# Performance work log

Hardware: AMD Instinct MI355X
Metric: run time of the kernel (lower is better)

Reference implementation:

```python
import jax, jax.numpy as jnp
import numpy as np

G = 56          # voxel grid resolution per axis
N = 65536
K = 27          # 3x3x3 kernel offsets
C_IN = 128
C_OUT = 128


def _build_rulebook():
    """Submanifold conv rulebook: for each kernel offset, (input_row, output_row) pairs.

    Padded to P=N pairs per offset; invalid pairs use in_idx=0 and out_idx=N
    (a dummy output slot that is dropped), so shapes are static.
    """
    rng = np.random.default_rng(0)
    keys = np.sort(rng.choice(G ** 3, size=N, replace=False)).astype(np.int64)
    x = keys // (G * G)
    y = (keys // G) % G
    z = keys % G
    in_idx = np.zeros((K, N), dtype=np.int32)
    out_idx = np.full((K, N), N, dtype=np.int32)
    k = 0
    for dx in (-1, 0, 1):
        for dy in (-1, 0, 1):
            for dz in (-1, 0, 1):
                nx, ny, nz = x + dx, y + dy, z + dz
                valid = (nx >= 0) & (nx < G) & (ny >= 0) & (ny < G) & (nz >= 0) & (nz < G)
                nkey = (nx * G + ny) * G + nz
                pos = np.searchsorted(keys, np.clip(nkey, 0, G ** 3 - 1))
                pos = np.clip(pos, 0, N - 1)
                found = valid & (keys[pos] == nkey)
                cnt = int(found.sum())
                in_idx[k, :cnt] = pos[found]
                out_idx[k, :cnt] = np.nonzero(found)[0]
                k += 1
    return jnp.asarray(in_idx), jnp.asarray(out_idx)


def setup_inputs() -> dict:
    key = jax.random.key(0)
    k1, k2, k3 = jax.random.split(key, 3)
    fan_in = K * C_IN
    features = jax.random.normal(k1, (N, C_IN), dtype=jnp.float32)
    weight = jax.random.normal(k2, (K, C_IN, C_OUT), dtype=jnp.float32) * (1.0 / np.sqrt(fan_in))
    bias = jax.random.normal(k3, (C_OUT,), dtype=jnp.float32) * 0.01
    in_idx, out_idx = _build_rulebook()
    return {"features": features, "weight": weight, "bias": bias,
            "in_idx": in_idx, "out_idx": out_idx}


def reference(features, weight, bias, in_idx, out_idx):
    # gather: [K, P, C_in]
    gathered = features[in_idx]
    # per-offset GEMM: [K, P, C_out]
    contrib = jnp.einsum('kpc,kcd->kpd', gathered, weight)
    n = features.shape[0]
    c_out = weight.shape[-1]
    # scatter-accumulate into N real rows + 1 dummy row for padded pairs
    out = jnp.zeros((n + 1, c_out), dtype=features.dtype)
    out = out.at[out_idx.reshape(-1)].add(contrib.reshape(-1, c_out))
    return out[:n] + bias
```

## Files before the change

kernel.cpp:

```cpp
#include <hip/hip_runtime.h>
#include <hip/hip_bf16.h>
#include <stdint.h>

#define NV   65536
#define KOFF 27
#define CIN  128
#define COUT 128

typedef __bf16 bf16x8 __attribute__((ext_vector_type(8)));
typedef float  f32x4  __attribute__((ext_vector_type(4)));

__device__ __forceinline__ void async_copy16(void* lds, const void* g) {
    __builtin_amdgcn_global_load_lds(
        (const __attribute__((address_space(1))) void*)g,
        (__attribute__((address_space(3))) void*)lds,
        16, 0, 0);
}

#define JOB_A_BLOCKS 4097
#define JOB_B_BLOCKS 216
#define JOB_S_BLOCKS 1728

__global__ void k_prep_all(const float* __restrict__ f,
                           uint4* __restrict__ fb4,
                           const float* __restrict__ w,
                           uint4* __restrict__ wfrag4,
                           const int4* __restrict__ in4,
                           const int4* __restrict__ out4,
                           int* __restrict__ nbr) {
    const int b = blockIdx.x;
    const int t = threadIdx.x;
    if (b < JOB_A_BLOCKS) {
        int i = b * 256 + t;
        int total8  = (NV + 1) * CIN / 8;
        int nvalid8 = NV * CIN / 8;
        if (i >= total8) return;
        union { uint4 u; __hip_bfloat16 h[8]; } p;
        if (i < nvalid8) {
            const float4* f4 = (const float4*)f;
            float4 a = f4[i * 2];
            float4 c = f4[i * 2 + 1];
            p.h[0] = __float2bfloat16(a.x);
            p.h[1] = __float2bfloat16(a.y);
            p.h[2] = __float2bfloat16(a.z);
            p.h[3] = __float2bfloat16(a.w);
            p.h[4] = __float2bfloat16(c.x);
            p.h[5] = __float2bfloat16(c.y);
            p.h[6] = __float2bfloat16(c.z);
            p.h[7] = __float2bfloat16(c.w);
        } else {
            p.u = make_uint4(0, 0, 0, 0);
        }
        fb4[i] = p.u;
    } else if (b < JOB_A_BLOCKS + JOB_B_BLOCKS) {
        int c    = (b - JOB_A_BLOCKS) * 256 + t;
        int lane = c & 63;
        int nt   = (c >> 6) & 1;
        int ks   = (c >> 7) & 3;
        int wv   = (c >> 9) & 3;
        int k    = c >> 11;
        int cout = wv * 32 + nt * 16 + (lane & 15);
        int cin0 = ks * 32 + (lane >> 4) * 8;
        const float* wk = w + k * 16384;
        union { uint4 u; __hip_bfloat16 h[8]; } p;
        #pragma unroll
        for (int j = 0; j < 8; ++j)
            p.h[j] = __float2bfloat16(wk[(cin0 + j) * 128 + cout]);
        wfrag4[c] = p.u;
    } else {
        int i = (b - JOB_A_BLOCKS - JOB_B_BLOCKS) * 256 + t;
        int k = i >> 14;
        int4 ii = in4[i];
        int4 oo = out4[i];
        int* nb = nbr + k * (NV + 1);
        nb[oo.x] = ii.x;
        nb[oo.y] = ii.y;
        nb[oo.z] = ii.z;
        nb[oo.w] = ii.w;
    }
}

__global__ __launch_bounds__(256, 2)
void sp_conv_main(const __hip_bfloat16* __restrict__ feats,
                  const uint4* __restrict__ wfrag,
                  const int* __restrict__ nbr,
                  const float* __restrict__ bias,
                  float* __restrict__ out) {
    __shared__ unsigned char smem[65536];

    const int t   = threadIdx.x;
    const int bid = blockIdx.x;
    const int tile0 = ((bid & 7) * 64 + (bid >> 3)) * 128;

    const int w    = t >> 6;
    const int lane = t & 63;
    const int lr   = lane & 15;
    const int quad = lane >> 4;

    const int srow   = t >> 4;
    const int sbyte  = ((t & 15) ^ srow) * 16;

    f32x4 acc[8][2] = {};

    const unsigned char* featsB = (const unsigned char*)feats;

    int arows[8];
    {
        const int* nbr0 = nbr + tile0;
        #pragma unroll
        for (int i = 0; i < 8; ++i) arows[i] = nbr0[i * 16 + srow];
    }
    #pragma unroll
    for (int i = 0; i < 8; ++i) {
        unsigned ar = min((unsigned)arows[i], (unsigned)NV);
        async_copy16(smem + i * 4096 + t * 16,
                     featsB + (size_t)ar * 256 + sbyte);
    }
    {
        const int* nbr1 = nbr + (NV + 1) + tile0;
        #pragma unroll
        for (int i = 0; i < 8; ++i) arows[i] = nbr1[i * 16 + srow];
    }
    uint4 bcur[4][2], bnext[4][2];
    {
        const uint4* wf0 = wfrag + w * 512 + lane;
        #pragma unroll
        for (int ks = 0; ks < 4; ++ks)
            #pragma unroll
            for (int nt = 0; nt < 2; ++nt)
                bcur[ks][nt] = wf0[ks * 128 + nt * 64];
    }
    __syncthreads();

    int cbuf = 0;
    for (int k = 0; k < KOFF; ++k) {
        if (k + 1 < KOFF) {
            unsigned char* dst = smem + (cbuf ^ 1) * 32768;
            #pragma unroll
            for (int i = 0; i < 8; ++i) {
                unsigned ar = min((unsigned)arows[i], (unsigned)NV);
                async_copy16(dst + i * 4096 + t * 16,
                             featsB + (size_t)ar * 256 + sbyte);
            }
            if (k + 2 < KOFF) {
                const int* nbrn = nbr + (k + 2) * (NV + 1) + tile0;
                #pragma unroll
                for (int i = 0; i < 8; ++i) arows[i] = nbrn[i * 16 + srow];
            }
            const uint4* wfn = wfrag + (k + 1) * 2048 + w * 512 + lane;
            #pragma unroll
            for (int ks = 0; ks < 4; ++ks)
                #pragma unroll
                for (int nt = 0; nt < 2; ++nt)
                    bnext[ks][nt] = wfn[ks * 128 + nt * 64];
        }

        const unsigned char* base = smem + cbuf * 32768;
        #pragma unroll
        for (int ks = 0; ks < 4; ++ks) {
            bf16x8 af[8];
            #pragma unroll
            for (int mt = 0; mt < 8; ++mt) {
                int row = mt * 16 + lr;
                af[mt] = *(const bf16x8*)(base + row * 256 +
                                          (((ks * 4 + quad) ^ lr) * 16));
            }
            #pragma unroll
            for (int mt = 0; mt < 8; ++mt)
                #pragma unroll
                for (int nt = 0; nt < 2; ++nt)
                    acc[mt][nt] = __builtin_amdgcn_mfma_f32_16x16x32_bf16(
                        af[mt], *(const bf16x8*)&bcur[ks][nt],
                        acc[mt][nt], 0, 0, 0);
        }
        __syncthreads();
        #pragma unroll
        for (int ks = 0; ks < 4; ++ks)
            #pragma unroll
            for (int nt = 0; nt < 2; ++nt)
                bcur[ks][nt] = bnext[ks][nt];
        cbuf ^= 1;
    }

    const int n0w = w * 32;
    float bv[2];
    #pragma unroll
    for (int nt = 0; nt < 2; ++nt) bv[nt] = bias[n0w + nt * 16 + lr];

    #pragma unroll
    for (int mt = 0; mt < 8; ++mt) {
        #pragma unroll
        for (int nt = 0; nt < 2; ++nt) {
            #pragma unroll
            for (int r = 0; r < 4; ++r) {
                int grow = tile0 + mt * 16 + quad * 4 + r;
                out[(size_t)grow * COUT + n0w + nt * 16 + lr] =
                    acc[mt][nt][r] + bv[nt];
            }
        }
    }
}


extern "C" void kernel_launch(void* const* d_in, const int* in_sizes, int n_in,
                              void* d_out, int out_size, void* d_ws, size_t ws_size,
                              hipStream_t stream) {
    const float* features = (const float*)d_in[0];
    const float* weight   = (const float*)d_in[1];
    const float* bias     = (const float*)d_in[2];
    const int*   in_idx   = (const int*)d_in[3];
    const int*   out_idx  = (const int*)d_in[4];
    float* out = (float*)d_out;

    uint8_t* ws = (uint8_t*)d_ws;
    size_t off = 0;
    __hip_bfloat16* feats_bf = (__hip_bfloat16*)(ws + off);
    off += (size_t)(NV + 1) * CIN * 2;
    off = (off + 255) & ~(size_t)255;
    uint4* wfrag = (uint4*)(ws + off);
    off += (size_t)KOFF * CIN * COUT * 2;
    off = (off + 255) & ~(size_t)255;
    int* nbr = (int*)(ws + off);

    hipMemsetAsync(nbr, 0xFF, (size_t)KOFF * (NV + 1) * 4, stream);

    k_prep_all<<<JOB_A_BLOCKS + JOB_B_BLOCKS + JOB_S_BLOCKS, 256, 0, stream>>>(
        features, (uint4*)feats_bf, weight, wfrag,
        (const int4*)in_idx, (const int4*)out_idx, nbr);

    sp_conv_main<<<NV / 128, 256, 0, stream>>>(feats_bf, wfrag, nbr, bias, out);
}
```

Baseline: 158.2 us.

## Split kernel offsets across three blocks per tile with atomic accumulation

Splits the 27 kernel offsets into three groups of nine. Each output tile is now handled by three blocks that write their partial sums into a zeroed output with float atomicAdd, and the first group adds the bias. This triples the grid from 512 blocks, which is meant to fill the many CUs better. The feature tile drops to a single 32KB LDS buffer so three blocks can fit per CU, and weight fragments are reordered and prefetched per k-slice in place of double-buffering whole offsets. The cost is an extra memset of the output, atomic traffic on 32MB of output, and lost overlap between the gather and the compute.

```diff
diff --git a/kernel.cpp b/kernel.cpp
--- a/kernel.cpp
+++ b/kernel.cpp
@@ -6,6 +6,8 @@
 #define KOFF 27
 #define CIN  128
 #define COUT 128
+#define NGRP 3
+#define KPG  9
 
 typedef __bf16 bf16x8 __attribute__((ext_vector_type(8)));
 typedef float  f32x4  __attribute__((ext_vector_type(4)));
@@ -56,9 +58,10 @@
         int c    = (b - JOB_A_BLOCKS) * 256 + t;
         int lane = c & 63;
         int nt   = (c >> 6) & 1;
-        int ks   = (c >> 7) & 3;
-        int wv   = (c >> 9) & 3;
-        int k    = c >> 11;
+        int wv   = (c >> 7) & 3;
+        int s    = c >> 9;
+        int ks   = s & 3;
+        int k    = s >> 2;
         int cout = wv * 32 + nt * 16 + (lane & 15);
         int cin0 = ks * 32 + (lane >> 4) * 8;
         const float* wk = w + k * 16384;
@@ -80,89 +83,83 @@
     }
 }
 
-__global__ __launch_bounds__(256, 2)
+__global__ __launch_bounds__(256, 3)
 void sp_conv_main(const __hip_bfloat16* __restrict__ feats,
                   const uint4* __restrict__ wfrag,
                   const int* __restrict__ nbr,
                   const float* __restrict__ bias,
                   float* __restrict__ out) {
-    __shared__ unsigned char smem[65536];
+    __shared__ unsigned char smA[32768];
 
     const int t   = threadIdx.x;
     const int bid = blockIdx.x;
-    const int tile0 = ((bid & 7) * 64 + (bid >> 3)) * 128;
+    const int g   = bid % NGRP;
+    const int tb  = bid / NGRP;
+    const int tile0 = ((tb & 7) * 64 + (tb >> 3)) * 128;
+    const int kbeg  = g * KPG;
+    const int send  = (kbeg + KPG) * 4;
 
     const int w    = t >> 6;
     const int lane = t & 63;
     const int lr   = lane & 15;
     const int quad = lane >> 4;
+    const int n0w  = w * 32;
 
     const int srow   = t >> 4;
     const int sbyte  = ((t & 15) ^ srow) * 16;
 
-    f32x4 acc[8][2] = {};
+    f32x4 acc[8][2];
+    {
+        float b0 = (g == 0) ? bias[n0w + lr]      : 0.0f;
+        float b1 = (g == 0) ? bias[n0w + 16 + lr] : 0.0f;
+        #pragma unroll
+        for (int mt = 0; mt < 8; ++mt) {
+            acc[mt][0] = (f32x4){b0, b0, b0, b0};
+            acc[mt][1] = (f32x4){b1, b1, b1, b1};
+        }
+    }
 
     const unsigned char* featsB = (const unsigned char*)feats;
 
     int arows[8];
     {
-        const int* nbr0 = nbr + tile0;
+        const int* nbr0 = nbr + kbeg * (NV + 1) + tile0;
         #pragma unroll
         for (int i = 0; i < 8; ++i) arows[i] = nbr0[i * 16 + srow];
     }
+    const uint4* wfp = wfrag + w * 128 + lane;
+    uint4 bb[2][2];
     #pragma unroll
-    for (int i = 0; i < 8; ++i) {
-        unsigned ar = min((unsigned)arows[i], (unsigned)NV);
-        async_copy16(smem + i * 4096 + t * 16,
-                     featsB + (size_t)ar * 256 + sbyte);
-    }
-    {
-        const int* nbr1 = nbr + (NV + 1) + tile0;
-        #pragma unroll
-        for (int i = 0; i < 8; ++i) arows[i] = nbr1[i * 16 + srow];
-    }
-    uint4 bcur[4][2], bnext[4][2];
-    {
-        const uint4* wf0 = wfrag + w * 512 + lane;
-        #pragma unroll
-        for (int ks = 0; ks < 4; ++ks)
-            #pragma unroll
-            for (int nt = 0; nt < 2; ++nt)
-                bcur[ks][nt] = wf0[ks * 128 + nt * 64];
-    }
-    __syncthreads();
-
-    int cbuf = 0;
-    for (int k = 0; k < KOFF; ++k) {
-        if (k + 1 < KOFF) {
-            unsigned char* dst = smem + (cbuf ^ 1) * 32768;
-            #pragma unroll
-            for (int i = 0; i < 8; ++i) {
-                unsigned ar = min((unsigned)arows[i], (unsigned)NV);
-                async_copy16(dst + i * 4096 + t * 16,
-                             featsB + (size_t)ar * 256 + sbyte);
-            }
-            if (k + 2 < KOFF) {
-                const int* nbrn = nbr + (k + 2) * (NV + 1) + tile0;
-                #pragma unroll
-                for (int i = 0; i < 8; ++i) arows[i] = nbrn[i * 16 + srow];
-            }
-            const uint4* wfn = wfrag + (k + 1) * 2048 + w * 512 + lane;
-            #pragma unroll
-            for (int ks = 0; ks < 4; ++ks)
+    for (int nt = 0; nt < 2; ++nt) bb[0][nt] = wfp[(size_t)(kbeg * 4) * 512 + nt * 64];
+
+    for (int k = kbeg; k < kbeg + KPG; ++k) {
+        #pragma unroll
+        for (int i = 0; i < 8; ++i) {
+            unsigned ar = min((unsigned)arows[i], (unsigned)NV);
+            async_copy16(smA + i * 4096 + t * 16,
+                         featsB + (size_t)ar * 256 + sbyte);
+        }
+        if (k + 1 < kbeg + KPG) {
+            const int* nbrn = nbr + (k + 1) * (NV + 1) + tile0;
+            #pragma unroll
+            for (int i = 0; i < 8; ++i) arows[i] = nbrn[i * 16 + srow];
+        }
+        __syncthreads();
+
+        #pragma unroll
+        for (int ks = 0; ks < 4; ++ks) {
+            const int s = k * 4 + ks;
+            if (s + 1 < send) {
+                const uint4* wfn = wfp + (size_t)(s + 1) * 512;
                 #pragma unroll
                 for (int nt = 0; nt < 2; ++nt)
-                    bnext[ks][nt] = wfn[ks * 128 + nt * 64];
-        }
-
-        const unsigned char* base = smem + cbuf * 32768;
-        #pragma unroll
-        for (int ks = 0; ks < 4; ++ks) {
+                    bb[(ks + 1) & 1][nt] = wfn[nt * 64];
+            }
             bf16x8 af[8];
             #pragma unroll
             for (int mt = 0; mt < 8; ++mt) {
                 int row = mt * 16 + lr;
-                af[mt] = *(const bf16x8*)(base + row * 256 +
+                af[mt] = *(const bf16x8*)(smA + row * 256 +
                                           (((ks * 4 + quad) ^ lr) * 16));
             }
             #pragma unroll
@@ -170,22 +167,11 @@
                 #pragma unroll
                 for (int nt = 0; nt < 2; ++nt)
                     acc[mt][nt] = __builtin_amdgcn_mfma_f32_16x16x32_bf16(
-                        af[mt], *(const bf16x8*)&bcur[ks][nt],
+                        af[mt], *(const bf16x8*)&bb[ks & 1][nt],
                         acc[mt][nt], 0, 0, 0);
         }
         __syncthreads();
-        #pragma unroll
-        for (int ks = 0; ks < 4; ++ks)
-            #pragma unroll
-            for (int nt = 0; nt < 2; ++nt)
-                bcur[ks][nt] = bnext[ks][nt];
-        cbuf ^= 1;
-    }
-
-    const int n0w = w * 32;
-    float bv[2];
-    #pragma unroll
-    for (int nt = 0; nt < 2; ++nt) bv[nt] = bias[n0w + nt * 16 + lr];
+    }
 
     #pragma unroll
     for (int mt = 0; mt < 8; ++mt) {
@@ -194,8 +180,8 @@
             #pragma unroll
             for (int r = 0; r < 4; ++r) {
                 int grow = tile0 + mt * 16 + quad * 4 + r;
-                out[(size_t)grow * COUT + n0w + nt * 16 + lr] =
-                    acc[mt][nt][r] + bv[nt];
+                atomicAdd(&out[(size_t)grow * COUT + n0w + nt * 16 + lr],
+                          acc[mt][nt][r]);
             }
         }
     }
@@ -218,15 +204,16 @@
     off += (size_t)(NV + 1) * CIN * 2;
     off = (off + 255) & ~(size_t)255;
     uint4* wfrag = (uint4*)(ws + off);
-    off += (size_t)KOFF * CIN * COUT * 2;
+    off += (size_t)108 * 512 * 16;
     off = (off + 255) & ~(size_t)255;
     int* nbr = (int*)(ws + off);
 
     hipMemsetAsync(nbr, 0xFF, (size_t)KOFF * (NV + 1) * 4, stream);
+    hipMemsetAsync(out, 0, (size_t)NV * COUT * 4, stream);
 
     k_prep_all<<<JOB_A_BLOCKS + JOB_B_BLOCKS + JOB_S_BLOCKS, 256, 0, stream>>>(
         features, (uint4*)feats_bf, weight, wfrag,
         (const int4*)in_idx, (const int4*)out_idx, nbr);
 
-    sp_conv_main<<<NV / 128, 256, 0, stream>>>(feats_bf, wfrag, nbr, bias, out);
-}
+    sp_conv_main<<<512 * NGRP, 256, 0, stream>>>(feats_bf, wfrag, nbr, bias, out);
+}
```

Measured after the change: 218.4 us. 1.38x slower.
